# Kernel optimization log

Hardware: AMD Instinct MI355X
Metric: run time of the kernel (lower is better)

Reference implementation:

```python
import jax, jax.numpy as jnp
import numpy as np

EMBED_DIM = 1024
NUM_HEAD = 16
HEAD_DIM = EMBED_DIM // NUM_HEAD


def _linear_params(key, in_dim, out_dim):
    kw, kb = jax.random.split(key)
    bound = 1.0 / np.sqrt(in_dim)
    W = jax.random.uniform(kw, (out_dim, in_dim), minval=-bound, maxval=bound, dtype=jnp.float32)
    b = jax.random.uniform(kb, (out_dim,), minval=-bound, maxval=bound, dtype=jnp.float32)
    return W, b


def setup_inputs() -> dict:
    key = jax.random.key(0)
    ks = jax.random.split(key, 7)
    N, S, E = 2, 2048, EMBED_DIM
    k = jax.random.normal(ks[0], (N, S, E), dtype=jnp.float32)
    q = jax.random.normal(ks[1], (N, S, E), dtype=jnp.float32)
    v = jax.random.normal(ks[2], (N, S, E), dtype=jnp.float32)
    Wk, bk = _linear_params(ks[3], E, E)
    Wq, bq = _linear_params(ks[4], E, E)
    Wv, bv = _linear_params(ks[5], E, E)
    Wo, bo = _linear_params(ks[6], E, E)
    return {"key": k, "query": q, "value": v,
            "Wk": Wk, "bk": bk, "Wq": Wq, "bq": bq,
            "Wv": Wv, "bv": bv, "Wo": Wo, "bo": bo}


def reference(key, query, value, Wk, bk, Wq, bq, Wv, bv, Wo, bo):
    N, S_in, E = key.shape
    S_out = query.shape[1]
    H, D = NUM_HEAD, HEAD_DIM
    # projections (torch Linear: x @ W.T + b), split heads -> [N, H, S, D]
    k = (key @ Wk.T + bk).reshape(N, S_in, H, D).transpose(0, 2, 1, 3)
    q = (query @ Wq.T + bq).reshape(N, S_out, H, D).transpose(0, 2, 1, 3)
    v = (value @ Wv.T + bv).reshape(N, S_in, H, D).transpose(0, 2, 1, 3)
    # unfused attention: full [N,H,S_out,S_in] score matrix, scale, softmax
    weight = jnp.einsum("nhqd,nhkd->nhqk", q, k) / jnp.sqrt(jnp.float32(D))
    weight = jax.nn.softmax(weight, axis=-1)
    attn = jnp.einsum("nhqk,nhkd->nhqd", weight, v)  # [N,H,S_out,D]
    attn = attn.transpose(0, 2, 1, 3).reshape(N, S_out, E)
    return attn @ Wo.T + bo
```

## Files before the change

kernel.cpp:

```cpp
#include <hip/hip_runtime.h>

constexpr int E  = 1024;
constexpr int NH = 16;
constexpr int HD = 64;
constexpr int S  = 2048;
constexpr int NB = 2;
constexpr int M  = NB * S;

typedef unsigned short u16;
typedef _Float16 f16;
typedef __attribute__((ext_vector_type(8))) _Float16 h8v;
typedef __attribute__((ext_vector_type(2))) __fp16 hp2v;
typedef __attribute__((ext_vector_type(4))) float f4v;

__device__ __forceinline__ f4v mfmaH(h8v a, h8v b, f4v c) {
    return __builtin_amdgcn_mfma_f32_16x16x32_f16(a, b, c, 0, 0, 0);
}
__device__ __forceinline__ u16 f16bits(float x) {
    union { f16 h; u16 u; } t; t.h = (f16)x; return t.u;
}
__device__ __forceinline__ unsigned pkrtz(float a, float b) {
    union { hp2v h; unsigned u; } t;
    t.h = __builtin_amdgcn_cvt_pkrtz(a, b);
    return t.u;
}
__device__ __forceinline__ float fexp2(float x) {
    float r;
    asm("v_exp_f32 %0, %1" : "=v"(r) : "v"(x));
    return r;
}
typedef const __attribute__((address_space(1))) void gvoid;
typedef __attribute__((address_space(3))) void lvoid;
__device__ __forceinline__ void load_lds16(const u16* g, u16* l) {
    __builtin_amdgcn_global_load_lds((gvoid*)g, (lvoid*)l, 16, 0, 0);
}

__global__ __launch_bounds__(256)
void cvt_f16(const float* __restrict__ wq, const float* __restrict__ wk,
             const float* __restrict__ wv, const float* __restrict__ wo,
             u16* __restrict__ out)
{
    const size_t EE = (size_t)E * E;
    const int z = blockIdx.y;
    const float* src = (z == 0) ? wq : (z == 1) ? wk : (z == 2) ? wv : wo;
    u16* dst = out + (size_t)z * EE;
    for (size_t i = ((size_t)blockIdx.x * 256 + threadIdx.x) * 8; i < EE;
         i += (size_t)gridDim.x * 256 * 8) {
        float4 a = *reinterpret_cast<const float4*>(src + i);
        float4 b = *reinterpret_cast<const float4*>(src + i + 4);
        h8v o;
        o[0] = (f16)a.x; o[1] = (f16)a.y; o[2] = (f16)a.z; o[3] = (f16)a.w;
        o[4] = (f16)b.x; o[5] = (f16)b.y; o[6] = (f16)b.z; o[7] = (f16)b.w;
        *reinterpret_cast<h8v*>(dst + i) = o;
    }
}

__device__ __forceinline__ void gemm16_core(const u16* __restrict__ A,
                                            const u16* __restrict__ W,
                                            int bm, int bn, u16* lds, f4v acc[4][4])
{
    const int tid  = threadIdx.x;
    const int lane = tid & 63;
    const int wid  = tid >> 6;
    const int g = lane >> 4, c = lane & 15;
    const int wr = wid >> 1, wc = wid & 1;
    const int lrow = lane >> 3;
    const int lslot = lane & 7;
    const int sslot = lslot ^ lrow;

    for (int k0 = 0; k0 < E; k0 += 64) {
        #pragma unroll
        for (int i = 0; i < 4; ++i) {
            int rbase = wid * 32 + i * 8;
            load_lds16(A + (size_t)(bm + rbase + lrow) * E + k0 + (sslot << 3),
                       &lds[rbase * 64]);
            load_lds16(W + (size_t)(bn + rbase + lrow) * E + k0 + (sslot << 3),
                       &lds[8192 + rbase * 64]);
        }
        __syncthreads();

        h8v a[4][2];
        #pragma unroll
        for (int mf = 0; mf < 4; ++mf) {
            int row = wr * 64 + mf * 16 + c;
            #pragma unroll
            for (int ks = 0; ks < 2; ++ks)
                a[mf][ks] = *reinterpret_cast<h8v*>(
                    &lds[row * 64 + ((((ks << 2) | g) ^ (c & 7)) << 3)]);
        }
        #pragma unroll
        for (int nf = 0; nf < 4; ++nf) {
            int row = wc * 64 + nf * 16 + c;
            #pragma unroll
            for (int ks = 0; ks < 2; ++ks) {
                h8v b = *reinterpret_cast<h8v*>(
                    &lds[8192 + row * 64 + ((((ks << 2) | g) ^ (c & 7)) << 3)]);
                #pragma unroll
                for (int mf = 0; mf < 4; ++mf)
                    acc[mf][nf] = mfmaH(a[mf][ks], b, acc[mf][nf]);
            }
        }
        __syncthreads();
    }
}

__device__ __forceinline__ void gemm16_core_mixed(const float* __restrict__ A,
                                                  const u16* __restrict__ W,
                                                  int bm, int bn, u16* lds,
                                                  f4v acc[4][4])
{
    const int tid  = threadIdx.x;
    const int lane = tid & 63;
    const int wid  = tid >> 6;
    const int g = lane >> 4, c = lane & 15;
    const int wr = wid >> 1, wc = wid & 1;
    const int lrow = lane >> 3;
    const int lslot = lane & 7;
    const int sslot = lslot ^ lrow;
    const int arow = tid >> 3;
    const int agrp = tid & 7;
    const int aswz = (agrp ^ (arow & 7)) << 3;

    for (int k0 = 0; k0 < E; k0 += 64) {
        #pragma unroll
        for (int i = 0; i < 4; ++i) {
            int rbase = wid * 32 + i * 8;
            load_lds16(W + (size_t)(bn + rbase + lrow) * E + k0 + (sslot << 3),
                       &lds[8192 + rbase * 64]);
        }
        #pragma unroll
        for (int i = 0; i < 4; ++i) {
            int row = arow + i * 32;
            const float* ap = &A[(size_t)(bm + row) * E + k0 + agrp * 8];
            float4 f0 = *reinterpret_cast<const float4*>(ap);
            float4 f1 = *reinterpret_cast<const float4*>(ap + 4);
            uint4 wv;
            wv.x = pkrtz(f0.x, f0.y); wv.y = pkrtz(f0.z, f0.w);
            wv.z = pkrtz(f1.x, f1.y); wv.w = pkrtz(f1.z, f1.w);
            *reinterpret_cast<uint4*>(&lds[row * 64 + aswz]) = wv;
        }
        __syncthreads();

        h8v a[4][2];
        #pragma unroll
        for (int mf = 0; mf < 4; ++mf) {
            int row = wr * 64 + mf * 16 + c;
            #pragma unroll
            for (int ks = 0; ks < 2; ++ks)
                a[mf][ks] = *reinterpret_cast<h8v*>(
                    &lds[row * 64 + ((((ks << 2) | g) ^ (c & 7)) << 3)]);
        }
        #pragma unroll
        for (int nf = 0; nf < 4; ++nf) {
            int row = wc * 64 + nf * 16 + c;
            #pragma unroll
            for (int ks = 0; ks < 2; ++ks) {
                h8v b = *reinterpret_cast<h8v*>(
                    &lds[8192 + row * 64 + ((((ks << 2) | g) ^ (c & 7)) << 3)]);
                #pragma unroll
                for (int mf = 0; mf < 4; ++mf)
                    acc[mf][nf] = mfmaH(a[mf][ks], b, acc[mf][nf]);
            }
        }
        __syncthreads();
    }
}

__global__ __launch_bounds__(256, 3)
void qkv_gemm(const float* __restrict__ query, const float* __restrict__ keyin,
              const float* __restrict__ value,
              const u16* __restrict__ wqf, const u16* __restrict__ wkf,
              const u16* __restrict__ wvf,
              const float* __restrict__ bq, const float* __restrict__ bk,
              const float* __restrict__ bv,
              u16* __restrict__ Qattn, u16* __restrict__ KV, float scaleQ)
{
    __shared__ __align__(16) u16 lds[16384];
    const int z = blockIdx.z;
    const float* A = (z == 0) ? query : (z == 1) ? keyin : value;
    const u16* W = (z == 0) ? wqf : (z == 1) ? wkf : wvf;
    const float* bias = (z == 0) ? bq : (z == 1) ? bk : bv;
    const float scl = (z == 0) ? scaleQ : 1.0f;
    const int bm = blockIdx.x * 128, bn = blockIdx.y * 128;

    f4v acc[4][4];
    #pragma unroll
    for (int a = 0; a < 4; ++a)
        #pragma unroll
        for (int b = 0; b < 4; ++b) acc[a][b] = (f4v){0.f, 0.f, 0.f, 0.f};

    gemm16_core_mixed(A, W, bm, bn, lds, acc);

    const int lane = threadIdx.x & 63;
    const int g = lane >> 4, c = lane & 15;
    const int wid = threadIdx.x >> 6;
    const int wr = wid >> 1, wc = wid & 1;
    float bcol[4];
    #pragma unroll
    for (int nf = 0; nf < 4; ++nf) bcol[nf] = bias[bn + wc * 64 + nf * 16 + c];

    #pragma unroll
    for (int mf = 0; mf < 4; ++mf)
        #pragma unroll
        for (int r = 0; r < 4; ++r) {
            int m  = bm + wr * 64 + mf * 16 + g * 4 + r;
            int nb = m >> 11, sp = m & (S - 1);
            #pragma unroll
            for (int nf = 0; nf < 4; ++nf) {
                int ncol = bn + wc * 64 + nf * 16 + c;
                int h = ncol >> 6, d = ncol & 63;
                int bh_ = nb * NH + h;
                u16 hb = f16bits((acc[mf][nf][r] + bcol[nf]) * scl);
                if (z == 0) {
                    Qattn[((size_t)bh_ * S + sp) * HD + d] = hb;
                } else if (z == 1) {
                    int t = sp >> 6, kk = (sp >> 4) & 3, cc = sp & 15;
                    int ds = d >> 5, gg = (d >> 3) & 3, j = d & 7;
                    KV[((size_t)bh_ * 32 + t) * 8192 +
                       ((size_t)((kk * 2 + ds) * 64 + gg * 16 + cc)) * 8 + j] = hb;
                } else {
                    int t = sp >> 6, rem = sp & 63;
                    int s2 = rem >> 5, bb = (rem >> 4) & 1, gg = (rem >> 2) & 3, a2 = rem & 3;
                    int j = 4 * bb + a2;
                    int df = d >> 4, cc = d & 15;
                    KV[((size_t)bh_ * 32 + t) * 8192 + 4096 +
                       ((size_t)((df * 2 + s2) * 64 + gg * 16 + cc)) * 8 + j] = hb;
                }
            }
        }
}

__global__ __launch_bounds__(256, 3)
void out_gemm(const u16* __restrict__ A, const u16* __restrict__ W,
              const float* __restrict__ bias, float* __restrict__ C)
{
    __shared__ __align__(16) u16 lds[16384];
    const int bm = blockIdx.x * 128, bn = blockIdx.y * 128;
    f4v acc[4][4];
    #pragma unroll
    for (int a = 0; a < 4; ++a)
        #pragma unroll
        for (int b = 0; b < 4; ++b) acc[a][b] = (f4v){0.f, 0.f, 0.f, 0.f};

    gemm16_core(A, W, bm, bn, lds, acc);

    const int lane = threadIdx.x & 63;
    const int g = lane >> 4, c = lane & 15;
    const int wid = threadIdx.x >> 6;
    const int wr = wid >> 1, wc = wid & 1;
    float bcol[4];
    #pragma unroll
    for (int nf = 0; nf < 4; ++nf) bcol[nf] = bias[bn + wc * 64 + nf * 16 + c];

    #pragma unroll
    for (int mf = 0; mf < 4; ++mf)
        #pragma unroll
        for (int r = 0; r < 4; ++r) {
            int m = bm + wr * 64 + mf * 16 + g * 4 + r;
            float* crow = &C[(size_t)m * E + bn + wc * 64];
            #pragma unroll
            for (int nf = 0; nf < 4; ++nf)
                crow[nf * 16 + c] = acc[mf][nf][r] + bcol[nf];
        }
}

__global__ __launch_bounds__(128, 2)
void attn_mfma(const u16* __restrict__ Qf, const u16* __restrict__ KV,
               u16* __restrict__ Out)
{
    __shared__ __align__(16) u16 lds[8192];
    const int tid  = threadIdx.x;
    const int lane = tid & 63;
    const int wid  = tid >> 6;
    const int g = lane >> 4, c = lane & 15;
    const int dlin = blockIdx.x;
    const int idx  = dlin >> 3;
    const int bh = (dlin & 7) * 4 + (idx >> 5);
    const int qc = idx & 31;
    const int n = bh >> 4, h = bh & 15;
    const int q0 = qc * 64 + wid * 32;
    const u16* kvb = KV + (size_t)bh * 32 * 8192;
    const f4v zero4 = {0.f, 0.f, 0.f, 0.f};

    h8v Qb[2][2];
    #pragma unroll
    for (int qf = 0; qf < 2; ++qf)
        #pragma unroll
        for (int ds = 0; ds < 2; ++ds)
            Qb[qf][ds] = *reinterpret_cast<const h8v*>(
                &Qf[((size_t)bh * S + q0 + qf * 16 + c) * HD + ds * 32 + g * 8]);

    h8v ones;
    #pragma unroll
    for (int i = 0; i < 8; ++i) ones[i] = (f16)1.0f;

    f4v oacc[2][4];
    #pragma unroll
    for (int qf = 0; qf < 2; ++qf)
        #pragma unroll
        for (int df = 0; df < 4; ++df) oacc[qf][df] = zero4;
    f4v lacc[2] = {zero4, zero4};

    f4v scA[2][4], scB[2][4];
    h8v vrA[4][2], vrB[4][2];

    #define STAGE_K(T, BUFOFF)                                                  \
    {                                                                           \
        const u16* src = kvb + (size_t)(T) * 8192 + wid * 2048 + lane * 8;      \
        u16* dst = &lds[(BUFOFF) + wid * 2048];                                 \
        _Pragma("unroll")                                                       \
        for (int i = 0; i < 4; ++i) load_lds16(src + i * 512, dst + i * 512);   \
    }
    #define VLOAD(T, VR)                                                        \
    {                                                                           \
        _Pragma("unroll")                                                       \
        for (int df = 0; df < 4; ++df)                                          \
            _Pragma("unroll")                                                   \
            for (int s2 = 0; s2 < 2; ++s2)                                      \
                VR[df][s2] = *reinterpret_cast<const h8v*>(                     \
                    &kvb[(size_t)(T) * 8192 + 4096 +                            \
                         ((size_t)((df * 2 + s2) * 64 + lane)) * 8]);           \
    }

    VLOAD(0, vrA);
    STAGE_K(0, 0);
    STAGE_K(1, 4096);

    asm volatile("s_waitcnt vmcnt(4)" ::: "memory");
    __builtin_amdgcn_s_barrier();
    {
        const u16* Bt = &lds[0];
        #pragma unroll
        for (int qf = 0; qf < 2; ++qf)
            #pragma unroll
            for (int kf = 0; kf < 4; ++kf) scA[qf][kf] = zero4;
        __builtin_amdgcn_s_setprio(1);
        #pragma unroll
        for (int kf = 0; kf < 4; ++kf)
            #pragma unroll
            for (int ds = 0; ds < 2; ++ds) {
                h8v kh = *reinterpret_cast<const h8v*>(
                    &Bt[((size_t)((kf * 2 + ds) * 64 + lane)) * 8]);
                #pragma unroll
                for (int qf = 0; qf < 2; ++qf)
                    scA[qf][kf] = mfmaH(kh, Qb[qf][ds], scA[qf][kf]);
            }
        __builtin_amdgcn_s_setprio(0);
        VLOAD(1, vrB);
    }
    __builtin_amdgcn_s_barrier();
    STAGE_K(2, 0);

    #define PHASE(T, BUFOFF, SCP, SCC, VOLD, WAITN)                             \
    asm volatile("s_waitcnt vmcnt(" WAITN ")" ::: "memory");                    \
    __builtin_amdgcn_s_barrier();                                               \
    {                                                                           \
        const u16* Bt = &lds[BUFOFF];                                           \
        _Pragma("unroll")                                                       \
        for (int qf = 0; qf < 2; ++qf)                                          \
            _Pragma("unroll")                                                   \
            for (int kf = 0; kf < 4; ++kf) SCC[qf][kf] = zero4;                 \
        __builtin_amdgcn_s_setprio(1);                                          \
        _Pragma("unroll")                                                       \
        for (int kf = 0; kf < 4; ++kf)                                          \
            _Pragma("unroll")                                                   \
            for (int ds = 0; ds < 2; ++ds) {                                    \
                h8v kh = *reinterpret_cast<const h8v*>(                         \
                    &Bt[((size_t)((kf * 2 + ds) * 64 + lane)) * 8]);            \
                _Pragma("unroll")                                               \
                for (int qf = 0; qf < 2; ++qf)                                  \
                    SCC[qf][kf] = mfmaH(kh, Qb[qf][ds], SCC[qf][kf]);           \
            }                                                                   \
        __builtin_amdgcn_s_setprio(0);                                          \
        h8v pah[2][2];                                                          \
        _Pragma("unroll")                                                       \
        for (int qf = 0; qf < 2; ++qf)                                          \
            _Pragma("unroll")                                                   \
            for (int s2 = 0; s2 < 2; ++s2) {                                    \
                union { h8v v; unsigned u[4]; } th;                             \
                _Pragma("unroll")                                               \
                for (int kfh = 0; kfh < 2; ++kfh) {                             \
                    int kf = 2 * s2 + kfh;                                      \
                    float p0 = fexp2(SCP[qf][kf][0]);                           \
                    float p1 = fexp2(SCP[qf][kf][1]);                           \
                    float p2 = fexp2(SCP[qf][kf][2]);                           \
                    float p3 = fexp2(SCP[qf][kf][3]);                           \
                    th.u[2 * kfh + 0] = pkrtz(p0, p1);                          \
                    th.u[2 * kfh + 1] = pkrtz(p2, p3);                          \
                }                                                               \
                pah[qf][s2] = th.v;                                             \
            }                                                                   \
        __builtin_amdgcn_s_setprio(1);                                          \
        _Pragma("unroll")                                                       \
        for (int qf = 0; qf < 2; ++qf) {                                        \
            lacc[qf] = mfmaH(pah[qf][0], ones, lacc[qf]);                       \
            lacc[qf] = mfmaH(pah[qf][1], ones, lacc[qf]);                       \
        }                                                                       \
        _Pragma("unroll")                                                       \
        for (int df = 0; df < 4; ++df)                                          \
            _Pragma("unroll")                                                   \
            for (int s2 = 0; s2 < 2; ++s2)                                      \
                _Pragma("unroll")                                               \
                for (int qf = 0; qf < 2; ++qf)                                  \
                    oacc[qf][df] = mfmaH(pah[qf][s2], VOLD[df][s2],             \
                                         oacc[qf][df]);                         \
        __builtin_amdgcn_s_setprio(0);                                          \
        if ((T) + 1 < 32) VLOAD((T) + 1, VOLD);                                 \
    }                                                                           \
    __builtin_amdgcn_s_barrier();                                               \
    if ((T) + 2 < 32) STAGE_K((T) + 2, BUFOFF)

    for (int t = 1; t < 31; t += 2) {
        PHASE(t,     4096, scA, scB, vrA, "12");
        PHASE(t + 1, 0,    scB, scA, vrB, "12");
    }
    PHASE(31, 4096, scA, scB, vrA, "8");
    #undef PHASE
    #undef STAGE_K
    #undef VLOAD

    {
        h8v pah[2][2];
        #pragma unroll
        for (int qf = 0; qf < 2; ++qf)
            #pragma unroll
            for (int s2 = 0; s2 < 2; ++s2) {
                union { h8v v; unsigned u[4]; } th;
                #pragma unroll
                for (int kfh = 0; kfh < 2; ++kfh) {
                    int kf = 2 * s2 + kfh;
                    float p0 = fexp2(scB[qf][kf][0]);
                    float p1 = fexp2(scB[qf][kf][1]);
                    float p2 = fexp2(scB[qf][kf][2]);
                    float p3 = fexp2(scB[qf][kf][3]);
                    th.u[2 * kfh + 0] = pkrtz(p0, p1);
                    th.u[2 * kfh + 1] = pkrtz(p2, p3);
                }
                pah[qf][s2] = th.v;
            }
        #pragma unroll
        for (int qf = 0; qf < 2; ++qf) {
            lacc[qf] = mfmaH(pah[qf][0], ones, lacc[qf]);
            lacc[qf] = mfmaH(pah[qf][1], ones, lacc[qf]);
        }
        #pragma unroll
        for (int df = 0; df < 4; ++df)
            #pragma unroll
            for (int s2 = 0; s2 < 2; ++s2)
                #pragma unroll
                for (int qf = 0; qf < 2; ++qf)
                    oacc[qf][df] = mfmaH(pah[qf][s2], vrB[df][s2], oacc[qf][df]);
    }

    #pragma unroll
    for (int qf = 0; qf < 2; ++qf)
        #pragma unroll
        for (int r = 0; r < 4; ++r) {
            float linv = 1.0f / lacc[qf][r];
            int q = q0 + qf * 16 + g * 4 + r;
            size_t ob = ((size_t)n * S + q) * E + h * HD;
            #pragma unroll
            for (int df = 0; df < 4; ++df)
                Out[ob + df * 16 + c] = f16bits(oacc[qf][df][r] * linv);
        }
}

extern "C" void kernel_launch(void* const* d_in, const int* in_sizes, int n_in,
                              void* d_out, int out_size, void* d_ws, size_t ws_size,
                              hipStream_t stream)
{
    const float* key   = (const float*)d_in[0];
    const float* query = (const float*)d_in[1];
    const float* value = (const float*)d_in[2];
    const float* Wk    = (const float*)d_in[3];
    const float* bk    = (const float*)d_in[4];
    const float* Wq    = (const float*)d_in[5];
    const float* bq    = (const float*)d_in[6];
    const float* Wv    = (const float*)d_in[7];
    const float* bv    = (const float*)d_in[8];
    const float* Wo    = (const float*)d_in[9];
    const float* bo    = (const float*)d_in[10];

    const size_t ME = (size_t)M * E, EE = (size_t)E * E;
    u16* ws16  = (u16*)d_ws;
    u16* wqf   = ws16;
    u16* wkf   = wqf + EE;
    u16* wvf   = wkf + EE;
    u16* wof   = wvf + EE;
    u16* Qattn = wof + EE;
    u16* KV    = Qattn + ME;
    u16* AoutH = KV + 2 * ME;

    const float SCALE_Q = 0.125f * 1.44269504088896340736f;

    cvt_f16<<<dim3(512, 4), 256, 0, stream>>>(Wq, Wk, Wv, Wo, ws16);
    qkv_gemm<<<dim3(M / 128, E / 128, 3), 256, 0, stream>>>(
        query, key, value, wqf, wkf, wvf, bq, bk, bv, Qattn, KV, SCALE_Q);
    attn_mfma<<<dim3((S / 64) * NB * NH), 128, 0, stream>>>(Qattn, KV, AoutH);
    out_gemm<<<dim3(M / 128, E / 128), 256, 0, stream>>>(AoutH, wof, bo, (float*)d_out);
}
```

Baseline: 117.2 us.

## Software-pipeline fp32 A loads into registers ahead of MFMA in QKV GEMM

Restructures the mixed-precision GEMM main loop so the next k-tile's fp32 activation loads are issued into registers before the current tile's MFMA compute. Explicit s_waitcnt vmcnt/lgkmcnt and raw s_barrier replace __syncthreads. The aim is to hide global load latency behind compute. In exchange it holds 32 more float registers under launch_bounds(256,3), and it relies on hand-counted vmcnt values that could be wrong if the compiler reorders or splits the loads.

Result: faster. 114.6 us, median of 2 (-2.2%).

```diff
diff --git a/kernel.cpp b/kernel.cpp
--- a/kernel.cpp
+++ b/kernel.cpp
@@ -121,49 +121,98 @@
     const int agrp = tid & 7;
     const int aswz = (agrp ^ (arow & 7)) << 3;
 
-    for (int k0 = 0; k0 < E; k0 += 64) {
-        #pragma unroll
-        for (int i = 0; i < 4; ++i) {
-            int rbase = wid * 32 + i * 8;
-            load_lds16(W + (size_t)(bn + rbase + lrow) * E + k0 + (sslot << 3),
-                       &lds[8192 + rbase * 64]);
-        }
-        #pragma unroll
-        for (int i = 0; i < 4; ++i) {
-            int row = arow + i * 32;
-            const float* ap = &A[(size_t)(bm + row) * E + k0 + agrp * 8];
-            float4 f0 = *reinterpret_cast<const float4*>(ap);
-            float4 f1 = *reinterpret_cast<const float4*>(ap + 4);
-            uint4 wv;
-            wv.x = pkrtz(f0.x, f0.y); wv.y = pkrtz(f0.z, f0.w);
-            wv.z = pkrtz(f1.x, f1.y); wv.w = pkrtz(f1.z, f1.w);
-            *reinterpret_cast<uint4*>(&lds[row * 64 + aswz]) = wv;
-        }
-        __syncthreads();
-
-        h8v a[4][2];
-        #pragma unroll
-        for (int mf = 0; mf < 4; ++mf) {
-            int row = wr * 64 + mf * 16 + c;
-            #pragma unroll
-            for (int ks = 0; ks < 2; ++ks)
-                a[mf][ks] = *reinterpret_cast<h8v*>(
-                    &lds[row * 64 + ((((ks << 2) | g) ^ (c & 7)) << 3)]);
-        }
-        #pragma unroll
-        for (int nf = 0; nf < 4; ++nf) {
-            int row = wc * 64 + nf * 16 + c;
-            #pragma unroll
-            for (int ks = 0; ks < 2; ++ks) {
-                h8v b = *reinterpret_cast<h8v*>(
-                    &lds[8192 + row * 64 + ((((ks << 2) | g) ^ (c & 7)) << 3)]);
-                #pragma unroll
-                for (int mf = 0; mf < 4; ++mf)
-                    acc[mf][nf] = mfmaH(a[mf][ks], b, acc[mf][nf]);
-            }
-        }
-        __syncthreads();
-    }
+    float4 af[4][2];
+
+    #define ALOAD(K0)                                                           \
+    {                                                                           \
+        _Pragma("unroll")                                                       \
+        for (int i = 0; i < 4; ++i) {                                           \
+            const float* ap = &A[(size_t)(bm + arow + i * 32) * E + (K0) + agrp * 8]; \
+            af[i][0] = *reinterpret_cast<const float4*>(ap);                    \
+            af[i][1] = *reinterpret_cast<const float4*>(ap + 4);                \
+        }                                                                       \
+    }
+    #define WSTAGE(K0)                                                          \
+    {                                                                           \
+        _Pragma("unroll")                                                       \
+        for (int i = 0; i < 4; ++i) {                                           \
+            int rbase = wid * 32 + i * 8;                                       \
+            load_lds16(W + (size_t)(bn + rbase + lrow) * E + (K0) + (sslot << 3),\
+                       &lds[8192 + rbase * 64]);                                \
+        }                                                                       \
+    }
+    #define AWRITE()                                                            \
+    {                                                                           \
+        _Pragma("unroll")                                                       \
+        for (int i = 0; i < 4; ++i) {                                           \
+            uint4 wv;                                                           \
+            wv.x = pkrtz(af[i][0].x, af[i][0].y);                               \
+            wv.y = pkrtz(af[i][0].z, af[i][0].w);                               \
+            wv.z = pkrtz(af[i][1].x, af[i][1].y);                               \
+            wv.w = pkrtz(af[i][1].z, af[i][1].w);                               \
+            *reinterpret_cast<uint4*>(&lds[(arow + i * 32) * 64 + aswz]) = wv;  \
+        }                                                                       \
+    }
+    #define GCOMPUTE()                                                          \
+    {                                                                           \
+        h8v a[4][2];                                                            \
+        _Pragma("unroll")                                                       \
+        for (int mf = 0; mf < 4; ++mf) {                                        \
+            int row = wr * 64 + mf * 16 + c;                                    \
+            _Pragma("unroll")                                                   \
+            for (int ks = 0; ks < 2; ++ks)                                      \
+                a[mf][ks] = *reinterpret_cast<h8v*>(                            \
+                    &lds[row * 64 + ((((ks << 2) | g) ^ (c & 7)) << 3)]);       \
+        }                                                                       \
+        _Pragma("unroll")                                                       \
+        for (int nf = 0; nf < 4; ++nf) {                                        \
+            int row = wc * 64 + nf * 16 + c;                                    \
+            _Pragma("unroll")                                                   \
+            for (int ks = 0; ks < 2; ++ks) {                                    \
+                h8v b = *reinterpret_cast<h8v*>(                                \
+                    &lds[8192 + row * 64 + ((((ks << 2) | g) ^ (c & 7)) << 3)]);\
+                _Pragma("unroll")                                               \
+                for (int mf = 0; mf < 4; ++mf)                                  \
+                    acc[mf][nf] = mfmaH(a[mf][ks], b, acc[mf][nf]);             \
+            }                                                                   \
+        }                                                                       \
+    }
+
+    ALOAD(0);
+    WSTAGE(0);
+    asm volatile("s_waitcnt vmcnt(4)" ::: "memory");
+    AWRITE();
+    ALOAD(64);
+    asm volatile("s_waitcnt lgkmcnt(0)" ::: "memory");
+    asm volatile("s_waitcnt vmcnt(8)" ::: "memory");
+    __builtin_amdgcn_s_barrier();
+    GCOMPUTE();
+
+    for (int k = 1; k < 15; ++k) {
+        __builtin_amdgcn_s_barrier();
+        WSTAGE(k * 64);
+        asm volatile("s_waitcnt vmcnt(4)" ::: "memory");
+        AWRITE();
+        ALOAD((k + 1) * 64);
+        asm volatile("s_waitcnt lgkmcnt(0)" ::: "memory");
+        asm volatile("s_waitcnt vmcnt(8)" ::: "memory");
+        __builtin_amdgcn_s_barrier();
+        GCOMPUTE();
+    }
+
+    __builtin_amdgcn_s_barrier();
+    WSTAGE(15 * 64);
+    asm volatile("s_waitcnt vmcnt(4)" ::: "memory");
+    AWRITE();
+    asm volatile("s_waitcnt lgkmcnt(0)" ::: "memory");
+    asm volatile("s_waitcnt vmcnt(0)" ::: "memory");
+    __builtin_amdgcn_s_barrier();
+    GCOMPUTE();
+
+    #undef ALOAD
+    #undef WSTAGE
+    #undef AWRITE
+    #undef GCOMPUTE
 }
 
 __global__ __launch_bounds__(256, 3)
```
